# Optimization experiments

Hardware: AMD Instinct MI355X
Metric: run time of the kernel (lower is better)

The kernel has to match this reference:

```python
import jax, jax.numpy as jnp
import numpy as np

N = 50000       # nodes
E = 800000      # edges (avg degree 16)
IN_DIM = 64
H = 64          # hidden_dim
OUT_DIM = 64
R = 8           # n_relations
L = 3           # n_layers
LN_EPS = 1e-5
NEG_SLOPE = 0.2


def _layer_norm(x, g, b):
    mu = jnp.mean(x, axis=-1, keepdims=True)
    var = jnp.mean((x - mu) ** 2, axis=-1, keepdims=True)
    return (x - mu) * jax.lax.rsqrt(var + LN_EPS) * g + b


def setup_inputs() -> dict:
    key = jax.random.key(0)
    ks = jax.random.split(key, 10)
    s = 0.05
    return {
        "x": jax.random.normal(ks[0], (N, IN_DIM), jnp.float32),
        "edge_index": jax.random.randint(ks[1], (2, E), 0, N),
        "edge_type": jax.random.randint(ks[2], (E,), 0, R),
        "W_in": jax.random.normal(ks[3], (H, IN_DIM), jnp.float32) * s,
        "b_in": jnp.zeros((H,), jnp.float32),
        "W_rel": jax.random.normal(ks[4], (R, H, H), jnp.float32) * s,   # no bias
        "W_gate": jax.random.normal(ks[5], (R, H, H), jnp.float32) * s,
        "b_gate": jnp.zeros((R, H), jnp.float32),
        "W_att": jax.random.normal(ks[6], (R, 2 * H), jnp.float32) * s,  # Linear(2H,1) per relation
        "b_att": jnp.zeros((R,), jnp.float32),
        "ln_gamma": jnp.ones((L, H), jnp.float32),
        "ln_beta": jnp.zeros((L, H), jnp.float32),
        "W_out": jax.random.normal(ks[7], (OUT_DIM, H), jnp.float32) * s,
        "b_out": jnp.zeros((OUT_DIM,), jnp.float32),
    }


def reference(x, edge_index, edge_type, W_in, b_in, W_rel, W_gate, b_gate,
              W_att, b_att, ln_gamma, ln_beta, W_out, b_out):
    src, dst = edge_index[0], edge_index[1]
    Wa_src, Wa_dst = W_att[:, :H], W_att[:, H:]      # [R,H] each
    seg = dst * R + edge_type                        # combined (node, relation) scatter key
    eidx = jnp.arange(E)

    h = jax.nn.relu(x @ W_in.T + b_in)               # [N,H]

    for layer in range(L):
        h_src = h[src]                               # [E,H] gather
        h_dst = h[dst]                               # [E,H] gather
        # attention score of each edge under its own relation's Linear(2H,1)
        scores_all = h_src @ Wa_src.T + h_dst @ Wa_dst.T + b_att   # [E,R]
        scores = scores_all[eidx, edge_type]                        # [E]
        scores = jax.nn.leaky_relu(scores, NEG_SLOPE)
        # softmax over dim=0 within each relation's edge set (as in the torch code)
        m = jax.ops.segment_max(scores, edge_type, num_segments=R)
        ex = jnp.exp(scores - m[edge_type])
        denom = jax.ops.segment_sum(ex, edge_type, num_segments=R)
        att = ex / denom[edge_type]                                 # [E]
        # relation-specific linear of source features (linear commutes with gather)
        hWr = jnp.einsum('nh,rkh->nrk', h, W_rel)                   # [N,R,H]
        msg = hWr[src, edge_type] * att[:, None]                    # [E,H]
        # per-relation scatter-add into destinations
        agg = jax.ops.segment_sum(msg, seg, num_segments=N * R)     # [N*R,H]
        agg = agg.reshape(N, R, H)
        gate = jax.nn.sigmoid(jnp.einsum('nh,rkh->nrk', h, W_gate) + b_gate)  # [N,R,H]
        h_new = jnp.mean(gate * agg, axis=1)         # sum(messages)/n_relations
        h = jax.nn.relu(_layer_norm(h + h_new, ln_gamma[layer], ln_beta[layer]))

    return h @ W_out.T + b_out
```

## Files before the change

### kernel.cpp

```cpp
#include <hip/hip_runtime.h>
#include <math.h>

#define NN 50000
#define EE 800000
#define HH 64
#define RR 8
#define LL 3
#define NR (NN * RR)
#define NB ((NR + 255) / 256)
#define LN_EPS 1e-5f
#define NEG_SLOPE 0.2f
#define LDH 68
#define PNB 584
#define OTB (16 * LDH)
#define DSPREAD 64

typedef __attribute__((ext_vector_type(8))) short bf8;
typedef __attribute__((ext_vector_type(4))) float f4;
typedef __attribute__((ext_vector_type(8))) unsigned short us8;
typedef __attribute__((ext_vector_type(2))) unsigned int u2;

__device__ __forceinline__ unsigned short bf16r(float f) {
    unsigned u = __float_as_uint(f);
    unsigned r = u + 0x7fffu + ((u >> 16) & 1u);
    return (unsigned short)(r >> 16);
}
__device__ __forceinline__ float bf2f(unsigned short u) {
    return __uint_as_float(((unsigned)u) << 16);
}

template<bool RELU>
__global__ void proj64(const float* __restrict__ in, const float* __restrict__ W,
                       const float* __restrict__ bias, float* __restrict__ out) {
    __shared__ float WT[64 * 65];
    __shared__ float xs[4 * 64];
    int tid = threadIdx.x;
    #pragma unroll
    for (int s = 0; s < 16; ++s) {
        int idx = tid + 256 * s;
        int k = idx >> 6, i = idx & 63;
        WT[i * 65 + k] = W[idx];
    }
    int w = tid >> 6, l = tid & 63;
    int n = blockIdx.x * 4 + w;
    if (n < NN) xs[w * 64 + l] = in[n * 64 + l];
    __syncthreads();
    if (n >= NN) return;
    float acc = 0.f;
    #pragma unroll
    for (int i = 0; i < 64; ++i) acc += xs[w * 64 + i] * WT[i * 65 + l];
    acc += bias[l];
    if (RELU) acc = fmaxf(acc, 0.f);
    out[n * 64 + l] = acc;
}

__global__ void att_pre(const float* __restrict__ h, const float* __restrict__ W_att,
                        float* __restrict__ s_src, float* __restrict__ s_dst,
                        unsigned short* __restrict__ hbf) {
    __shared__ float hs[32 * 65];
    __shared__ float was[8 * 65];
    __shared__ float wad[8 * 65];
    int tid = threadIdx.x;
    int n0 = blockIdx.x * 32;
    #pragma unroll
    for (int s = 0; s < 4; ++s) {
        int idx = tid + 256 * s;
        int r = idx >> 7, c = idx & 127;
        float v = W_att[idx];
        if (c < 64) was[r * 65 + c] = v;
        else        wad[r * 65 + (c - 64)] = v;
    }
    #pragma unroll
    for (int s = 0; s < 8; ++s) {
        int idx = tid + 256 * s;
        int nl = idx >> 6, c = idx & 63;
        int n = n0 + nl;
        float v = 0.f;
        if (n < NN) {
            v = h[(size_t)n * 64 + c];
            hbf[(size_t)n * 64 + c] = bf16r(v);
        }
        hs[nl * 65 + c] = v;
    }
    __syncthreads();
    int nl = tid >> 3, r = tid & 7;
    int n = n0 + nl;
    if (n >= NN) return;
    float as = 0.f, ad = 0.f;
    #pragma unroll
    for (int k = 0; k < 64; ++k) {
        float hv = hs[nl * 65 + k];
        as += hv * was[r * 65 + k];
        ad += hv * wad[r * 65 + k];
    }
    s_src[n * 8 + r] = as;
    s_dst[n * 8 + r] = ad;
}

__global__ void edge_count(const int* __restrict__ ei, const int* __restrict__ et,
                           int* __restrict__ counts, int* __restrict__ rank) {
    int e = blockIdx.x * 256 + threadIdx.x;
    int d = ei[EE + e], t = et[e];
    rank[e] = atomicAdd(&counts[d * 8 + t], 1);
}

__global__ void scan1(const int* __restrict__ counts, int* __restrict__ offs,
                      int* __restrict__ bsum) {
    __shared__ int s[256];
    int tid = threadIdx.x;
    int i = blockIdx.x * 256 + tid;
    int v = (i < NR) ? counts[i] : 0;
    s[tid] = v; __syncthreads();
    for (int d = 1; d < 256; d <<= 1) {
        int x = (tid >= d) ? s[tid - d] : 0;
        __syncthreads();
        s[tid] += x;
        __syncthreads();
    }
    if (i < NR) offs[i] = s[tid] - v;
    if (tid == 255) bsum[blockIdx.x] = s[255];
}

__global__ void scan2(int* __restrict__ bsum) {
    __shared__ int s[256];
    int tid = threadIdx.x;
    int carry = 0;
    for (int c0 = 0; c0 < NB; c0 += 256) {
        int i = c0 + tid;
        int v = (i < NB) ? bsum[i] : 0;
        s[tid] = v; __syncthreads();
        for (int d = 1; d < 256; d <<= 1) {
            int x = (tid >= d) ? s[tid - d] : 0;
            __syncthreads();
            s[tid] += x;
            __syncthreads();
        }
        if (i < NB) bsum[i] = carry + s[tid] - v;
        int tot = s[255];
        __syncthreads();
        carry += tot;
    }
}

__global__ void scan3(int* __restrict__ offs, const int* __restrict__ bsum) {
    int i = blockIdx.x * 256 + threadIdx.x;
    if (i < NR) offs[i] += bsum[i >> 8];
}

__global__ void edge_fill(const int* __restrict__ ei, const int* __restrict__ et,
                          const int* __restrict__ rank, const int* __restrict__ offs,
                          u2* __restrict__ spack) {
    int e = blockIdx.x * 256 + threadIdx.x;
    int s = ei[e], d = ei[EE + e], t = et[e];
    int seg = d * 8 + t;
    int slot = offs[seg] + rank[e];
    spack[slot] = (u2){(unsigned)s, (unsigned)seg};
}

__global__ void cvt_w(const float* __restrict__ Wr, const float* __restrict__ Wg,
                      const float* __restrict__ Wa,
                      unsigned short* __restrict__ WrB, unsigned short* __restrict__ WgB,
                      unsigned short* __restrict__ WaB) {
    int i = blockIdx.x * 256 + threadIdx.x;
    WrB[i] = bf16r(Wr[i]);
    WgB[i] = bf16r(Wg[i]);
    if (i < 1024) {
        int row = i >> 6, k = i & 63;
        float v = (row < 8) ? Wa[row * 128 + k] : Wa[(row - 8) * 128 + 64 + k];
        WaB[i] = bf16r(v);
    }
}

__global__ void edge_softmax2(const u2* __restrict__ spack,
                              const float* __restrict__ s_src, const float* __restrict__ s_dst,
                              const float* __restrict__ b_att,
                              u2* __restrict__ epack, float* __restrict__ dpart) {
    __shared__ float lsum[4][8];
    int tid = threadIdx.x;
    if (tid < 32) lsum[tid >> 3][tid & 7] = 0.f;
    __syncthreads();
    int slot = blockIdx.x * 256 + tid;
    u2 sp = spack[slot];
    int src = (int)sp[0];
    int seg = (int)sp[1];
    int t = seg & 7;
    float sc = s_src[src * 8 + t] + s_dst[seg] + b_att[t];
    sc = (sc >= 0.f) ? sc : NEG_SLOPE * sc;
    float ex = __expf(sc);
    epack[slot] = (u2){(unsigned)src, __float_as_uint(ex)};
    atomicAdd(&lsum[tid >> 6][t], ex);
    __syncthreads();
    if (tid < 8) {
        float v = lsum[0][tid] + lsum[1][tid] + lsum[2][tid] + lsum[3][tid];
        atomicAdd(&dpart[(blockIdx.x & (DSPREAD - 1)) * 16 + tid], v);
    }
}

__global__ void reduce_denom(float* __restrict__ dpart, float* __restrict__ denomL) {
    int tid = threadIdx.x;
    if (tid < 8) {
        float s = 0.f;
        #pragma unroll 8
        for (int j = 0; j < DSPREAD; ++j) s += dpart[j * 16 + tid];
        denomL[tid] = s;
    }
    __syncthreads();
    for (int i = tid; i < DSPREAD * 16; i += 64) dpart[i] = 0.f;
}

template<bool EMIT>
__global__ __launch_bounds__(256, 5) void combine_fused(
    const float* __restrict__ hbuf, const unsigned short* __restrict__ hbf_in,
    const int* __restrict__ offs, const u2* __restrict__ epack,
    const float* __restrict__ denomL,
    const unsigned short* __restrict__ WrB, const unsigned short* __restrict__ WgB,
    const unsigned short* __restrict__ WaB, const float* __restrict__ b_gate,
    const float* __restrict__ gamma, const float* __restrict__ beta,
    float* __restrict__ hout, unsigned short* __restrict__ hbf_out,
    float* __restrict__ ssrc_out, float* __restrict__ sdst_out) {
    __shared__ float hs[16 * LDH];
    __shared__ alignas(16) unsigned short ps[16 * PNB];
    __shared__ float idn8[8];
    __shared__ int offsL[129];
    float* ps_f = (float*)ps;
    int tid = threadIdx.x;
    int n0 = blockIdx.x * 16;

    {
        int row = tid >> 4, c4 = tid & 15;
        f4 v = ((const f4*)hbuf)[(size_t)(n0 + row) * 16 + c4];
        *(f4*)&hs[row * LDH + c4 * 4] = v;
    }
    if (tid < 129) {
        int sidx = n0 * 8 + tid;
        offsL[tid] = (sidx < NR) ? offs[sidx] : EE;
    }
    if (tid < 8) idn8[tid] = 1.f / denomL[tid];
    __syncthreads();

    {
        int segl = tid >> 1;
        int half = tid & 1;
        int lo = offsL[segl], hi = offsL[segl + 1];
        int r = segl & 7;
        int gn = segl >> 3;
        float fa[32];
        #pragma unroll
        for (int j = 0; j < 32; ++j) fa[j] = 0.f;
        for (int s = lo; s < hi; ++s) {
            u2 pk = epack[s];
            int src = (int)pk[0];
            float a = __uint_as_float(pk[1]);
            const us8* hp = (const us8*)(hbf_in + ((size_t)src << 6) + half * 32);
            #pragma unroll
            for (int q = 0; q < 4; ++q) {
                us8 hv = hp[q];
                #pragma unroll
                for (int j = 0; j < 8; ++j)
                    fa[q * 8 + j] += a * bf2f(hv[j]);
            }
        }
        float sA = idn8[r];
        unsigned short* pp = &ps[gn * PNB + r * 72 + half * 32];
        #pragma unroll
        for (int q = 0; q < 4; ++q) {
            us8 o;
            #pragma unroll
            for (int j = 0; j < 8; ++j) o[j] = bf16r(fa[q * 8 + j] * sA);
            *(us8*)(pp + q * 8) = o;
        }
    }
    __syncthreads();

    int w = tid >> 6, lane = tid & 63;
    int quad = lane >> 4, lr = lane & 15;
    int tn = w;

    bf8 a_h[2];
    #pragma unroll
    for (int kb = 0; kb < 2; ++kb) {
        const float* p = &hs[lr * LDH + kb * 32 + quad * 8];
        bf8 a;
        #pragma unroll
        for (int j = 0; j < 8; ++j) a[j] = (short)bf16r(p[j]);
        a_h[kb] = a;
    }

    f4 acc = (f4){0.f, 0.f, 0.f, 0.f};
    for (int r = 0; r < 8; ++r) {
        bf8 a_p[2];
        #pragma unroll
        for (int kb = 0; kb < 2; ++kb)
            a_p[kb] = *(const bf8*)&ps[lr * PNB + r * 72 + kb * 32 + quad * 8];
        f4 aggc = (f4){0.f, 0.f, 0.f, 0.f};
        f4 gacc = (f4){0.f, 0.f, 0.f, 0.f};
        #pragma unroll
        for (int kb = 0; kb < 2; ++kb) {
            const bf8* br = (const bf8*)(WrB + ((r * 64 + tn * 16 + lr) * 64 + kb * 32 + quad * 8));
            const bf8* bg = (const bf8*)(WgB + ((r * 64 + tn * 16 + lr) * 64 + kb * 32 + quad * 8));
            aggc = __builtin_amdgcn_mfma_f32_16x16x32_bf16(a_p[kb], *br, aggc, 0, 0, 0);
            gacc = __builtin_amdgcn_mfma_f32_16x16x32_bf16(a_h[kb], *bg, gacc, 0, 0, 0);
        }
        float bg = b_gate[r * 64 + tn * 16 + lr];
        #pragma unroll
        for (int j = 0; j < 4; ++j) {
            float g = 1.f / (1.f + __expf(-(gacc[j] + bg)));
            acc[j] += g * aggc[j];
        }
    }
    __syncthreads();

    #pragma unroll
    for (int j = 0; j < 4; ++j) {
        int row = quad * 4 + j;
        int col = tn * 16 + lr;
        ps_f[row * LDH + col] = hs[row * LDH + col] + acc[j] * 0.125f;
    }
    __syncthreads();

    {
        int row = tid >> 4, c = tid & 15;
        int n = n0 + row;
        f4 tv = *(const f4*)&ps_f[row * LDH + c * 4];
        float s1 = tv[0] + tv[1] + tv[2] + tv[3];
        float s2 = tv[0]*tv[0] + tv[1]*tv[1] + tv[2]*tv[2] + tv[3]*tv[3];
        #pragma unroll
        for (int off = 1; off <= 8; off <<= 1) {
            s1 += __shfl_xor(s1, off, 64);
            s2 += __shfl_xor(s2, off, 64);
        }
        float mu = s1 * (1.f / 64.f);
        float var = s2 * (1.f / 64.f) - mu * mu;
        float rs = rsqrtf(var + LN_EPS);
        f4 g = *(const f4*)(gamma + c * 4);
        f4 b = *(const f4*)(beta + c * 4);
        f4 ov;
        #pragma unroll
        for (int j = 0; j < 4; ++j)
            ov[j] = fmaxf((tv[j] - mu) * rs * g[j] + b[j], 0.f);
        *(f4*)(hout + (size_t)n * 64 + c * 4) = ov;
        if (EMIT) {
            *(f4*)&ps_f[OTB + row * LDH + c * 4] = ov;
            u2 u;
            u[0] = (unsigned)bf16r(ov[0]) | ((unsigned)bf16r(ov[1]) << 16);
            u[1] = (unsigned)bf16r(ov[2]) | ((unsigned)bf16r(ov[3]) << 16);
            *(u2*)(hbf_out + (size_t)n * 64 + c * 4) = u;
        }
    }

    if (EMIT) {
        __syncthreads();
        if (w == 0) {
            f4 sc = (f4){0.f, 0.f, 0.f, 0.f};
            #pragma unroll
            for (int kb = 0; kb < 2; ++kb) {
                const float* p = &ps_f[OTB + lr * LDH + kb * 32 + quad * 8];
                bf8 a;
                #pragma unroll
                for (int j = 0; j < 8; ++j) a[j] = (short)bf16r(p[j]);
                const bf8* bw = (const bf8*)(WaB + lr * 64 + kb * 32 + quad * 8);
                sc = __builtin_amdgcn_mfma_f32_16x16x32_bf16(a, *bw, sc, 0, 0, 0);
            }
            #pragma unroll
            for (int j = 0; j < 4; ++j) {
                int n = n0 + quad * 4 + j;
                if (lr < 8) ssrc_out[n * 8 + lr] = sc[j];
                else        sdst_out[n * 8 + (lr - 8)] = sc[j];
            }
        }
    }
}

extern "C" void kernel_launch(void* const* d_in, const int* in_sizes, int n_in,
                              void* d_out, int out_size, void* d_ws, size_t ws_size,
                              hipStream_t stream) {
    const float* x      = (const float*)d_in[0];
    const int*   ei     = (const int*)d_in[1];
    const int*   et     = (const int*)d_in[2];
    const float* W_in   = (const float*)d_in[3];
    const float* b_in   = (const float*)d_in[4];
    const float* W_rel  = (const float*)d_in[5];
    const float* W_gate = (const float*)d_in[6];
    const float* b_gate = (const float*)d_in[7];
    const float* W_att  = (const float*)d_in[8];
    const float* b_att  = (const float*)d_in[9];
    const float* ln_g   = (const float*)d_in[10];
    const float* ln_b   = (const float*)d_in[11];
    const float* W_out  = (const float*)d_in[12];
    const float* b_out  = (const float*)d_in[13];
    float* out = (float*)d_out;

    float* h0 = (float*)d_out;

    char* ws = (char*)d_ws;
    float* h1 = (float*)ws;                     ws += (size_t)NN * 64 * 4;
    unsigned short* hbfA = (unsigned short*)ws; ws += (size_t)NN * 64 * 2;
    unsigned short* hbfB = (unsigned short*)ws; ws += (size_t)NN * 64 * 2;
    float* s_src = (float*)ws;                  ws += (size_t)NN * 8 * 4;
    float* s_dst = (float*)ws;                  ws += (size_t)NN * 8 * 4;
    unsigned short* WrB = (unsigned short*)ws;  ws += (size_t)RR * 64 * 64 * 2;
    unsigned short* WgB = (unsigned short*)ws;  ws += (size_t)RR * 64 * 64 * 2;
    unsigned short* WaB = (unsigned short*)ws;  ws += 2048;
    int* counts = (int*)ws;                     ws += (size_t)NR * 4;
    float* denoms = (float*)ws;                 ws += 128;
    float* dpart = (float*)ws;                  ws += DSPREAD * 16 * 4;
    int* offs = (int*)ws;                       ws += (size_t)NR * 4;
    int* bsum = (int*)ws;                       ws += 6400;
    int* rank = (int*)ws;                       ws += (size_t)EE * 4;
    u2* spack = (u2*)ws;                        ws += (size_t)EE * 8;
    u2* epack = (u2*)ws;                        ws += (size_t)EE * 8;

    hipMemsetAsync(counts, 0, (size_t)NR * 4 + 128 + DSPREAD * 16 * 4, stream);
    cvt_w<<<128, 256, 0, stream>>>(W_rel, W_gate, W_att, WrB, WgB, WaB);
    edge_count<<<EE / 256, 256, 0, stream>>>(ei, et, counts, rank);
    scan1<<<NB, 256, 0, stream>>>(counts, offs, bsum);
    scan2<<<1, 256, 0, stream>>>(bsum);
    scan3<<<NB, 256, 0, stream>>>(offs, bsum);
    edge_fill<<<EE / 256, 256, 0, stream>>>(ei, et, rank, offs, spack);
    proj64<true><<<(NN + 3) / 4, 256, 0, stream>>>(x, W_in, b_in, h0);
    att_pre<<<(NN + 31) / 32, 256, 0, stream>>>(h0, W_att, s_src, s_dst, hbfA);

    const int tiles16 = NN / 16;
    float* hA = h0;  float* hB = h1;
    unsigned short* bfA = hbfA;  unsigned short* bfB = hbfB;
    for (int layer = 0; layer < LL; ++layer) {
        edge_softmax2<<<EE / 256, 256, 0, stream>>>(spack, s_src, s_dst, b_att,
                                                    epack, dpart);
        reduce_denom<<<1, 64, 0, stream>>>(dpart, denoms + 8 * layer);
        if (layer < LL - 1) {
            combine_fused<true><<<tiles16, 256, 0, stream>>>(
                hA, bfA, offs, epack, denoms + 8 * layer,
                WrB, WgB, WaB, b_gate, ln_g + layer * 64, ln_b + layer * 64,
                hB, bfB, s_src, s_dst);
        } else {
            combine_fused<false><<<tiles16, 256, 0, stream>>>(
                hA, bfA, offs, epack, denoms + 8 * layer,
                WrB, WgB, WaB, b_gate, ln_g + layer * 64, ln_b + layer * 64,
                hB, bfB, s_src, s_dst);
        }
        float* tf = hA; hA = hB; hB = tf;
        unsigned short* tb = bfA; bfA = bfB; bfB = tb;
    }
    proj64<false><<<(NN + 3) / 4, 256, 0, stream>>>(hA, W_out, b_out, out);
}
```

Baseline: 460.5 us.

## Fuse input projection with attention prep, output proj into last layer, drop small kernels

Merges the input projection with the attention-score precompute and bf16 conversion into one kernel, using wave shuffles. Folds the output projection into the last combine kernel as a bf16 MFMA, and drops scan3 and reduce_denom by applying block offsets and summing denominator partials inside the consumers, with per-layer partial buffers. Also widens scan2 to 1024 threads, processes two edges per gather iteration for more memory-level parallelism, and raises the launch-bounds occupancy hint from 5 to 8. This cuts launches and intermediate round trips, at the cost of more register pressure and a bf16 output projection.

```diff
diff --git a/kernel.cpp b/kernel.cpp
--- a/kernel.cpp
+++ b/kernel.cpp
@@ -29,9 +29,10 @@
     return __uint_as_float(((unsigned)u) << 16);
 }
 
-template<bool RELU>
-__global__ void proj64(const float* __restrict__ in, const float* __restrict__ W,
-                       const float* __restrict__ bias, float* __restrict__ out) {
+__global__ void proj_in(const float* __restrict__ x, const float* __restrict__ W,
+                        const float* __restrict__ bias, const float* __restrict__ W_att,
+                        float* __restrict__ h, unsigned short* __restrict__ hbf,
+                        float* __restrict__ s_src, float* __restrict__ s_dst) {
     __shared__ float WT[64 * 65];
     __shared__ float xs[4 * 64];
     int tid = threadIdx.x;
@@ -43,58 +44,33 @@
     }
     int w = tid >> 6, l = tid & 63;
     int n = blockIdx.x * 4 + w;
-    if (n < NN) xs[w * 64 + l] = in[n * 64 + l];
-    __syncthreads();
-    if (n >= NN) return;
+    xs[w * 64 + l] = x[(size_t)n * 64 + l];
+    __syncthreads();
     float acc = 0.f;
     #pragma unroll
     for (int i = 0; i < 64; ++i) acc += xs[w * 64 + i] * WT[i * 65 + l];
     acc += bias[l];
-    if (RELU) acc = fmaxf(acc, 0.f);
-    out[n * 64 + l] = acc;
-}
-
-__global__ void att_pre(const float* __restrict__ h, const float* __restrict__ W_att,
-                        float* __restrict__ s_src, float* __restrict__ s_dst,
-                        unsigned short* __restrict__ hbf) {
-    __shared__ float hs[32 * 65];
-    __shared__ float was[8 * 65];
-    __shared__ float wad[8 * 65];
-    int tid = threadIdx.x;
-    int n0 = blockIdx.x * 32;
-    #pragma unroll
-    for (int s = 0; s < 4; ++s) {
-        int idx = tid + 256 * s;
-        int r = idx >> 7, c = idx & 127;
-        float v = W_att[idx];
-        if (c < 64) was[r * 65 + c] = v;
-        else        wad[r * 65 + (c - 64)] = v;
-    }
-    #pragma unroll
-    for (int s = 0; s < 8; ++s) {
-        int idx = tid + 256 * s;
-        int nl = idx >> 6, c = idx & 63;
-        int n = n0 + nl;
-        float v = 0.f;
-        if (n < NN) {
-            v = h[(size_t)n * 64 + c];
-            hbf[(size_t)n * 64 + c] = bf16r(v);
-        }
-        hs[nl * 65 + c] = v;
-    }
-    __syncthreads();
-    int nl = tid >> 3, r = tid & 7;
-    int n = n0 + nl;
-    if (n >= NN) return;
-    float as = 0.f, ad = 0.f;
-    #pragma unroll
-    for (int k = 0; k < 64; ++k) {
-        float hv = hs[nl * 65 + k];
-        as += hv * was[r * 65 + k];
-        ad += hv * wad[r * 65 + k];
-    }
-    s_src[n * 8 + r] = as;
-    s_dst[n * 8 + r] = ad;
+    acc = fmaxf(acc, 0.f);
+    h[(size_t)n * 64 + l] = acc;
+    hbf[(size_t)n * 64 + l] = bf16r(acc);
+    float wsrc[8], wdst[8];
+    #pragma unroll
+    for (int r = 0; r < 8; ++r) {
+        wsrc[r] = W_att[r * 128 + l];
+        wdst[r] = W_att[r * 128 + 64 + l];
+    }
+    #pragma unroll
+    for (int r = 0; r < 8; ++r) {
+        float v = acc * wsrc[r];
+        float u = acc * wdst[r];
+        #pragma unroll
+        for (int off = 1; off <= 32; off <<= 1) {
+            v += __shfl_xor(v, off, 64);
+            u += __shfl_xor(u, off, 64);
+        }
+        if (l == r) s_src[n * 8 + r] = v;
+        if (l == 8 + r) s_dst[n * 8 + r] = u;
+    }
 }
 
 __global__ void edge_count(const int* __restrict__ ei, const int* __restrict__ et,
@@ -122,45 +98,40 @@
 }
 
 __global__ void scan2(int* __restrict__ bsum) {
-    __shared__ int s[256];
+    __shared__ int s[1024];
     int tid = threadIdx.x;
     int carry = 0;
-    for (int c0 = 0; c0 < NB; c0 += 256) {
+    for (int c0 = 0; c0 < NB; c0 += 1024) {
         int i = c0 + tid;
         int v = (i < NB) ? bsum[i] : 0;
         s[tid] = v; __syncthreads();
-        for (int d = 1; d < 256; d <<= 1) {
+        for (int d = 1; d < 1024; d <<= 1) {
             int x = (tid >= d) ? s[tid - d] : 0;
             __syncthreads();
             s[tid] += x;
             __syncthreads();
         }
         if (i < NB) bsum[i] = carry + s[tid] - v;
-        int tot = s[255];
+        int tot = s[1023];
         __syncthreads();
         carry += tot;
     }
 }
 
-__global__ void scan3(int* __restrict__ offs, const int* __restrict__ bsum) {
-    int i = blockIdx.x * 256 + threadIdx.x;
-    if (i < NR) offs[i] += bsum[i >> 8];
-}
-
 __global__ void edge_fill(const int* __restrict__ ei, const int* __restrict__ et,
                           const int* __restrict__ rank, const int* __restrict__ offs,
-                          u2* __restrict__ spack) {
+                          const int* __restrict__ bsum, u2* __restrict__ spack) {
     int e = blockIdx.x * 256 + threadIdx.x;
     int s = ei[e], d = ei[EE + e], t = et[e];
     int seg = d * 8 + t;
-    int slot = offs[seg] + rank[e];
+    int slot = offs[seg] + bsum[seg >> 8] + rank[e];
     spack[slot] = (u2){(unsigned)s, (unsigned)seg};
 }
 
 __global__ void cvt_w(const float* __restrict__ Wr, const float* __restrict__ Wg,
-                      const float* __restrict__ Wa,
+                      const float* __restrict__ Wa, const float* __restrict__ Wo,
                       unsigned short* __restrict__ WrB, unsigned short* __restrict__ WgB,
-                      unsigned short* __restrict__ WaB) {
+                      unsigned short* __restrict__ WaB, unsigned short* __restrict__ WoB) {
     int i = blockIdx.x * 256 + threadIdx.x;
     WrB[i] = bf16r(Wr[i]);
     WgB[i] = bf16r(Wg[i]);
@@ -169,6 +140,7 @@
         float v = (row < 8) ? Wa[row * 128 + k] : Wa[(row - 8) * 128 + 64 + k];
         WaB[i] = bf16r(v);
     }
+    if (i < 4096) WoB[i] = bf16r(Wo[i]);
 }
 
 __global__ void edge_softmax2(const u2* __restrict__ spack,
@@ -196,28 +168,18 @@
     }
 }
 
-__global__ void reduce_denom(float* __restrict__ dpart, float* __restrict__ denomL) {
-    int tid = threadIdx.x;
-    if (tid < 8) {
-        float s = 0.f;
-        #pragma unroll 8
-        for (int j = 0; j < DSPREAD; ++j) s += dpart[j * 16 + tid];
-        denomL[tid] = s;
-    }
-    __syncthreads();
-    for (int i = tid; i < DSPREAD * 16; i += 64) dpart[i] = 0.f;
-}
-
-template<bool EMIT>
-__global__ __launch_bounds__(256, 5) void combine_fused(
+template<bool EMIT, bool OUT>
+__global__ __launch_bounds__(256, 8) void combine_fused(
     const float* __restrict__ hbuf, const unsigned short* __restrict__ hbf_in,
-    const int* __restrict__ offs, const u2* __restrict__ epack,
-    const float* __restrict__ denomL,
+    const int* __restrict__ offs, const int* __restrict__ bsum,
+    const u2* __restrict__ epack, const float* __restrict__ dpartL,
     const unsigned short* __restrict__ WrB, const unsigned short* __restrict__ WgB,
-    const unsigned short* __restrict__ WaB, const float* __restrict__ b_gate,
-    const float* __restrict__ gamma, const float* __restrict__ beta,
-    float* __restrict__ hout, unsigned short* __restrict__ hbf_out,
-    float* __restrict__ ssrc_out, float* __restrict__ sdst_out) {
+    const unsigned short* __restrict__ WaB, const unsigned short* __restrict__ WoB,
+    const float* __restrict__ b_gate, const float* __restrict__ gamma,
+    const float* __restrict__ beta, float* __restrict__ hout,
+    unsigned short* __restrict__ hbf_out, float* __restrict__ ssrc_out,
+    float* __restrict__ sdst_out, float* __restrict__ outp,
+    const float* __restrict__ b_out) {
     __shared__ float hs[16 * LDH];
     __shared__ alignas(16) unsigned short ps[16 * PNB];
     __shared__ float idn8[8];
@@ -233,9 +195,18 @@
     }
     if (tid < 129) {
         int sidx = n0 * 8 + tid;
-        offsL[tid] = (sidx < NR) ? offs[sidx] : EE;
-    }
-    if (tid < 8) idn8[tid] = 1.f / denomL[tid];
+        offsL[tid] = (sidx < NR) ? (offs[sidx] + bsum[sidx >> 8]) : EE;
+    }
+    if (tid < 64) {
+        int t = tid & 7, g = tid >> 3;
+        float sm = 0.f;
+        #pragma unroll
+        for (int j = 0; j < 8; ++j) sm += dpartL[(g * 8 + j) * 16 + t];
+        sm += __shfl_xor(sm, 8, 64);
+        sm += __shfl_xor(sm, 16, 64);
+        sm += __shfl_xor(sm, 32, 64);
+        if (tid < 8) idn8[t] = 1.f / sm;
+    }
     __syncthreads();
 
     {
@@ -247,17 +218,23 @@
         float fa[32];
         #pragma unroll
         for (int j = 0; j < 32; ++j) fa[j] = 0.f;
-        for (int s = lo; s < hi; ++s) {
-            u2 pk = epack[s];
-            int src = (int)pk[0];
-            float a = __uint_as_float(pk[1]);
-            const us8* hp = (const us8*)(hbf_in + ((size_t)src << 6) + half * 32);
+        for (int s = lo; s < hi; s += 2) {
+            u2 pk0 = epack[s];
+            int s1 = (s + 1 < hi) ? (s + 1) : s;
+            u2 pk1 = epack[s1];
+            float a0 = __uint_as_float(pk0[1]);
+            float a1 = (s + 1 < hi) ? __uint_as_float(pk1[1]) : 0.f;
+            const us8* hp0 = (const us8*)(hbf_in + ((size_t)(int)pk0[0] << 6) + half * 32);
+            const us8* hp1 = (const us8*)(hbf_in + ((size_t)(int)pk1[0] << 6) + half * 32);
             #pragma unroll
             for (int q = 0; q < 4; ++q) {
-                us8 hv = hp[q];
+                us8 v0 = hp0[q];
+                us8 v1 = hp1[q];
                 #pragma unroll
-                for (int j = 0; j < 8; ++j)
-                    fa[q * 8 + j] += a * bf2f(hv[j]);
+                for (int j = 0; j < 8; ++j) {
+                    fa[q * 8 + j] += a0 * bf2f(v0[j]);
+                    fa[q * 8 + j] += a1 * bf2f(v1[j]);
+                }
             }
         }
         float sA = idn8[r];
@@ -338,9 +315,10 @@
         #pragma unroll
         for (int j = 0; j < 4; ++j)
             ov[j] = fmaxf((tv[j] - mu) * rs * g[j] + b[j], 0.f);
-        *(f4*)(hout + (size_t)n * 64 + c * 4) = ov;
+        if (!OUT)
+            *(f4*)(hout + (size_t)n * 64 + c * 4) = ov;
+        *(f4*)&ps_f[OTB + row * LDH + c * 4] = ov;
         if (EMIT) {
-            *(f4*)&ps_f[OTB + row * LDH + c * 4] = ov;
             u2 u;
             u[0] = (unsigned)bf16r(ov[0]) | ((unsigned)bf16r(ov[1]) << 16);
             u[1] = (unsigned)bf16r(ov[2]) | ((unsigned)bf16r(ov[3]) << 16);
@@ -369,6 +347,24 @@
             }
         }
     }
+
+    if (OUT) {
+        __syncthreads();
+        f4 oc = (f4){0.f, 0.f, 0.f, 0.f};
+        #pragma unroll
+        for (int kb = 0; kb < 2; ++kb) {
+            const float* p = &ps_f[OTB + lr * LDH + kb * 32 + quad * 8];
+            bf8 a;
+            #pragma unroll
+            for (int j = 0; j < 8; ++j) a[j] = (short)bf16r(p[j]);
+            const bf8* bw = (const bf8*)(WoB + ((tn * 16 + lr) * 64 + kb * 32 + quad * 8));
+            oc = __builtin_amdgcn_mfma_f32_16x16x32_bf16(a, *bw, oc, 0, 0, 0);
+        }
+        float bo = b_out[tn * 16 + lr];
+        #pragma unroll
+        for (int j = 0; j < 4; ++j)
+            outp[(size_t)(n0 + quad * 4 + j) * 64 + tn * 16 + lr] = oc[j] + bo;
+    }
 }
 
 extern "C" void kernel_launch(void* const* d_in, const int* in_sizes, int n_in,
@@ -401,45 +397,42 @@
     unsigned short* WrB = (unsigned short*)ws;  ws += (size_t)RR * 64 * 64 * 2;
     unsigned short* WgB = (unsigned short*)ws;  ws += (size_t)RR * 64 * 64 * 2;
     unsigned short* WaB = (unsigned short*)ws;  ws += 2048;
+    unsigned short* WoB = (unsigned short*)ws;  ws += 8192;
     int* counts = (int*)ws;                     ws += (size_t)NR * 4;
-    float* denoms = (float*)ws;                 ws += 128;
-    float* dpart = (float*)ws;                  ws += DSPREAD * 16 * 4;
+    float* dpart = (float*)ws;                  ws += 3 * DSPREAD * 16 * 4;
     int* offs = (int*)ws;                       ws += (size_t)NR * 4;
     int* bsum = (int*)ws;                       ws += 6400;
     int* rank = (int*)ws;                       ws += (size_t)EE * 4;
     u2* spack = (u2*)ws;                        ws += (size_t)EE * 8;
     u2* epack = (u2*)ws;                        ws += (size_t)EE * 8;
 
-    hipMemsetAsync(counts, 0, (size_t)NR * 4 + 128 + DSPREAD * 16 * 4, stream);
-    cvt_w<<<128, 256, 0, stream>>>(W_rel, W_gate, W_att, WrB, WgB, WaB);
+    hipMemsetAsync(counts, 0, (size_t)NR * 4 + 3 * DSPREAD * 16 * 4, stream);
+    cvt_w<<<128, 256, 0, stream>>>(W_rel, W_gate, W_att, W_out, WrB, WgB, WaB, WoB);
     edge_count<<<EE / 256, 256, 0, stream>>>(ei, et, counts, rank);
     scan1<<<NB, 256, 0, stream>>>(counts, offs, bsum);
-    scan2<<<1, 256, 0, stream>>>(bsum);
-    scan3<<<NB, 256, 0, stream>>>(offs, bsum);
-    edge_fill<<<EE / 256, 256, 0, stream>>>(ei, et, rank, offs, spack);
-    proj64<true><<<(NN + 3) / 4, 256, 0, stream>>>(x, W_in, b_in, h0);
-    att_pre<<<(NN + 31) / 32, 256, 0, stream>>>(h0, W_att, s_src, s_dst, hbfA);
+    scan2<<<1, 1024, 0, stream>>>(bsum);
+    edge_fill<<<EE / 256, 256, 0, stream>>>(ei, et, rank, offs, bsum, spack);
+    proj_in<<<NN / 4, 256, 0, stream>>>(x, W_in, b_in, W_att, h0, hbfA, s_src, s_dst);
 
     const int tiles16 = NN / 16;
     float* hA = h0;  float* hB = h1;
     unsigned short* bfA = hbfA;  unsigned short* bfB = hbfB;
     for (int layer = 0; layer < LL; ++layer) {
+        float* dpl = dpart + (size_t)layer * DSPREAD * 16;
         edge_softmax2<<<EE / 256, 256, 0, stream>>>(spack, s_src, s_dst, b_att,
-                                                    epack, dpart);
-        reduce_denom<<<1, 64, 0, stream>>>(dpart, denoms + 8 * layer);
+                                                    epack, dpl);
         if (layer < LL - 1) {
-            combine_fused<true><<<tiles16, 256, 0, stream>>>(
-                hA, bfA, offs, epack, denoms + 8 * layer,
-                WrB, WgB, WaB, b_gate, ln_g + layer * 64, ln_b + layer * 64,
-                hB, bfB, s_src, s_dst);
+            combine_fused<true, false><<<tiles16, 256, 0, stream>>>(
+                hA, bfA, offs, bsum, epack, dpl, WrB, WgB, WaB, WoB, b_gate,
+                ln_g + layer * 64, ln_b + layer * 64,
+                hB, bfB, s_src, s_dst, out, b_out);
         } else {
-            combine_fused<false><<<tiles16, 256, 0, stream>>>(
-                hA, bfA, offs, epack, denoms + 8 * layer,
-                WrB, WgB, WaB, b_gate, ln_g + layer * 64, ln_b + layer * 64,
-                hB, bfB, s_src, s_dst);
+            combine_fused<false, true><<<tiles16, 256, 0, stream>>>(
+                hA, bfA, offs, bsum, epack, dpl, WrB, WgB, WaB, WoB, b_gate,
+                ln_g + layer * 64, ln_b + layer * 64,
+                hB, bfB, s_src, s_dst, out, b_out);
         }
         float* tf = hA; hA = hB; hB = tf;
         unsigned short* tb = bfA; bfA = bfB; bfB = tb;
     }
-    proj64<false><<<(NN + 3) / 4, 256, 0, stream>>>(hA, W_out, b_out, out);
-}
+}
```

New measurement: 468.2 us. Within noise of the previous version (+1.7%).
